# Performance work log

Measured on AMD Instinct MI355X. Metric: run time of the kernel, lower is better.

Reference implementation:

```python
import jax, jax.numpy as jnp
import numpy as np

B, H, W, C = 32, 64, 64, 256


def setup_inputs() -> dict:
    key = jax.random.key(0)
    kq, kk, kv = jax.random.split(key, 3)
    query = jax.random.normal(kq, (B, H, W, C), dtype=jnp.float32)
    keys = jax.random.normal(kk, (B, H, W, C), dtype=jnp.float32)
    values = jax.random.normal(kv, (B, H, W, C), dtype=jnp.float32)
    return {"query": query, "keys": keys, "values": values}


def reference(query, keys, values):
    # A[b,q,k] = sum_{h,w} query[b,h,w,q] * keys[b,h,w,k]
    scores = jnp.einsum("bhwq,bhwk->bqk", query, keys)
    attn = jax.nn.softmax(scores, axis=-1)  # softmax over keys axis
    # out[b,q,h,w] = sum_k attn[b,q,k] * values[b,h,w,k]
    out = jnp.einsum("bqk,bhwk->bqhw", attn, values)
    return out
```

## Files before the change

kernel.cpp:

```cpp
#include <hip/hip_runtime.h>
#include <hip/hip_bf16.h>

#define B_  32
#define HW_ 4096
#define C_  256
#define S_LDS 40

using bf16x8 = __attribute__((ext_vector_type(8))) short;
using f32x4  = __attribute__((ext_vector_type(4))) float;

__device__ __forceinline__ ushort f2bf_rn(float x) {
    uint u = __builtin_bit_cast(uint, x);
    u += 0x7FFFu + ((u >> 16) & 1u);
    return (ushort)(u >> 16);
}
__device__ __forceinline__ uint pk_bf2(float a, float b) {
    return ((uint)f2bf_rn(b) << 16) | (uint)f2bf_rn(a);
}
__device__ __forceinline__ uint pk_rtz(float x0, float x1) {
    return __builtin_amdgcn_perm(__builtin_bit_cast(uint, x1),
                                 __builtin_bit_cast(uint, x0), 0x07060302u);
}
__device__ __forceinline__ void split2_rtz(float x0, float x1, uint& hi2, uint& lo2) {
    uint u0 = __builtin_bit_cast(uint, x0), u1 = __builtin_bit_cast(uint, x1);
    hi2 = __builtin_amdgcn_perm(u1, u0, 0x07060302u);
    float h0 = __builtin_bit_cast(float, u0 & 0xFFFF0000u);
    float h1 = __builtin_bit_cast(float, u1 & 0xFFFF0000u);
    lo2 = pk_rtz(x0 - h0, x1 - h1);
}

__global__ __launch_bounds__(256) void scores_kernel(const float* __restrict__ qg,
                                                     const float* __restrict__ kg,
                                                     float* __restrict__ scores) {
    int x  = blockIdx.x;
    int s  = x & 3;
    int tn = (x >> 2) & 3;
    int tm = (x >> 4) & 1;
    int b  = x >> 5;

    __shared__ __align__(16) ushort Qhi[128 * S_LDS], Qlo[128 * S_LDS];
    __shared__ __align__(16) ushort Khi[64 * S_LDS],  Klo[64 * S_LDS];

    int tid = threadIdx.x, lane = tid & 63, w = tid >> 6;
    int m0 = (w >> 1) * 64;
    int n0 = (w & 1) * 32;
    int g = lane >> 4, r16 = lane & 15;

    int cq = tid & 127;
    int hq = (tid >> 7) * 16;
    int ck = tid & 63;
    int hk = (tid >> 6) * 8;

    const float* qcol = qg + (size_t)b * HW_ * C_ + tm * 128 + cq;
    const float* kcol = kg + (size_t)b * HW_ * C_ + tn * 64 + ck;

    f32x4 acc[4][2];
#pragma unroll
    for (int i = 0; i < 4; ++i)
#pragma unroll
        for (int j = 0; j < 2; ++j) acc[i][j] = (f32x4){0.f, 0.f, 0.f, 0.f};

#define LOAD_QK(qr, kr, itv) {                                                 \
        int hw0 = s * 1024 + (itv) * 32;                                       \
        const float* qp = qcol + (size_t)(hw0 + hq) * C_;                      \
        _Pragma("unroll")                                                      \
        for (int j = 0; j < 16; ++j) qr[j] = qp[(size_t)j * C_];               \
        const float* kp = kcol + (size_t)(hw0 + hk) * C_;                      \
        _Pragma("unroll")                                                      \
        for (int j = 0; j < 8; ++j) kr[j] = kp[(size_t)j * C_];                \
    }

#define CONVERT_STORE(qr, kr) {                                                \
        uint qh[8], ql[8];                                                     \
        _Pragma("unroll")                                                      \
        for (int p = 0; p < 8; ++p) split2_rtz(qr[2*p], qr[2*p+1], qh[p], ql[p]); \
        int qb_ = cq * S_LDS + hq;                                             \
        *reinterpret_cast<uint4*>(&Qhi[qb_])     = make_uint4(qh[0], qh[1], qh[2], qh[3]); \
        *reinterpret_cast<uint4*>(&Qhi[qb_ + 8]) = make_uint4(qh[4], qh[5], qh[6], qh[7]); \
        *reinterpret_cast<uint4*>(&Qlo[qb_])     = make_uint4(ql[0], ql[1], ql[2], ql[3]); \
        *reinterpret_cast<uint4*>(&Qlo[qb_ + 8]) = make_uint4(ql[4], ql[5], ql[6], ql[7]); \
        uint kh[4], kl[4];                                                     \
        _Pragma("unroll")                                                      \
        for (int p = 0; p < 4; ++p) split2_rtz(kr[2*p], kr[2*p+1], kh[p], kl[p]); \
        int kb_ = ck * S_LDS + hk;                                             \
        *reinterpret_cast<uint4*>(&Khi[kb_]) = make_uint4(kh[0], kh[1], kh[2], kh[3]); \
        *reinterpret_cast<uint4*>(&Klo[kb_]) = make_uint4(kl[0], kl[1], kl[2], kl[3]); \
    }

#define MFMA_PHASE() {                                                         \
        bf16x8 ahi[4], alo[4];                                                 \
        _Pragma("unroll")                                                      \
        for (int mi = 0; mi < 4; ++mi) {                                       \
            int off = (m0 + mi * 16 + r16) * S_LDS + g * 8;                    \
            ahi[mi] = *reinterpret_cast<const bf16x8*>(&Qhi[off]);             \
            alo[mi] = *reinterpret_cast<const bf16x8*>(&Qlo[off]);             \
        }                                                                      \
        _Pragma("unroll")                                                      \
        for (int ni = 0; ni < 2; ++ni) {                                       \
            int off = (n0 + ni * 16 + r16) * S_LDS + g * 8;                    \
            bf16x8 bhi = *reinterpret_cast<const bf16x8*>(&Khi[off]);          \
            bf16x8 blo = *reinterpret_cast<const bf16x8*>(&Klo[off]);          \
            _Pragma("unroll")                                                  \
            for (int mi = 0; mi < 4; ++mi) {                                   \
                acc[mi][ni] = __builtin_amdgcn_mfma_f32_16x16x32_bf16(ahi[mi], bhi, acc[mi][ni], 0, 0, 0); \
                acc[mi][ni] = __builtin_amdgcn_mfma_f32_16x16x32_bf16(ahi[mi], blo, acc[mi][ni], 0, 0, 0); \
                acc[mi][ni] = __builtin_amdgcn_mfma_f32_16x16x32_bf16(alo[mi], bhi, acc[mi][ni], 0, 0, 0); \
            }                                                                  \
        }                                                                      \
    }

#define STEP(qc, kc, qn, kn, itv, doload) {                                    \
        if (doload) LOAD_QK(qn, kn, (itv) + 1);                                \
        __syncthreads();                                                       \
        CONVERT_STORE(qc, kc);                                                 \
        __syncthreads();                                                       \
        MFMA_PHASE();                                                          \
    }

    float qa[16], ka[8], qb[16], kb[8];
    LOAD_QK(qa, ka, 0);
    for (int p = 0; p < 16; ++p) {
        STEP(qa, ka, qb, kb, 2 * p, true);
        STEP(qb, kb, qa, ka, 2 * p + 1, p < 15);
    }

#pragma unroll
    for (int mi = 0; mi < 4; ++mi)
#pragma unroll
        for (int ni = 0; ni < 2; ++ni)
#pragma unroll
            for (int r = 0; r < 4; ++r) {
                int qrow = tm * 128 + m0 + mi * 16 + g * 4 + r;
                int kc   = tn * 64 + n0 + ni * 16 + r16;
                atomicAdd(&scores[((size_t)b * 256 + qrow) * 256 + kc], acc[mi][ni][r]);
            }
#undef STEP
#undef MFMA_PHASE
#undef CONVERT_STORE
#undef LOAD_QK
}

__global__ __launch_bounds__(256) void softmax_kernel(const float* __restrict__ scores,
                                                      ushort* __restrict__ attn) {
    int wid  = blockIdx.x * 4 + (threadIdx.x >> 6);
    int lane = threadIdx.x & 63;
    const float4 v = *reinterpret_cast<const float4*>(scores + (size_t)wid * 256 + lane * 4);
    float m = fmaxf(fmaxf(v.x, v.y), fmaxf(v.z, v.w));
#pragma unroll
    for (int off = 32; off; off >>= 1) m = fmaxf(m, __shfl_xor(m, off, 64));
    float e0 = __expf(v.x - m), e1 = __expf(v.y - m), e2 = __expf(v.z - m), e3 = __expf(v.w - m);
    float ssum = e0 + e1 + e2 + e3;
#pragma unroll
    for (int off = 32; off; off >>= 1) ssum += __shfl_xor(ssum, off, 64);
    float inv = 1.0f / ssum;
    uint2 o;
    o.x = pk_bf2(e0 * inv, e1 * inv);
    o.y = pk_bf2(e2 * inv, e3 * inv);
    *reinterpret_cast<uint2*>(attn + (size_t)wid * 256 + lane * 4) = o;
}

__global__ __launch_bounds__(256) void pv_kernel(const ushort* __restrict__ attn,
                                                 const float* __restrict__ vg,
                                                 float* __restrict__ out) {
    int b   = blockIdx.x >> 6;
    int hw0 = (blockIdx.x & 63) * 64;
    int tid = threadIdx.x, lane = tid & 63, w = tid >> 6;
    int m0  = w * 64;
    int g   = lane >> 4, r16 = lane & 15;

    f32x4 acc[4][4];
#pragma unroll
    for (int i = 0; i < 4; ++i)
#pragma unroll
        for (int j = 0; j < 4; ++j) acc[i][j] = (f32x4){0.f, 0.f, 0.f, 0.f};

    for (int ks = 0; ks < 8; ++ks) {
        int k0 = ks * 32;
        bf16x8 a[4];
#pragma unroll
        for (int mi = 0; mi < 4; ++mi) {
            int qrow = m0 + mi * 16 + r16;
            a[mi] = *reinterpret_cast<const bf16x8*>(attn + ((size_t)b * 256 + qrow) * 256 + k0 + g * 8);
        }
        float4 vv[4][2];
#pragma unroll
        for (int ni = 0; ni < 4; ++ni) {
            int hw = hw0 + ni * 16 + r16;
            const float* vp = vg + ((size_t)(b * HW_ + hw)) * C_ + k0 + g * 8;
            vv[ni][0] = *reinterpret_cast<const float4*>(vp);
            vv[ni][1] = *reinterpret_cast<const float4*>(vp + 4);
        }
#pragma unroll
        for (int ni = 0; ni < 4; ++ni) {
            bf16x8 bf;
            uint* bu = reinterpret_cast<uint*>(&bf);
            bu[0] = pk_rtz(vv[ni][0].x, vv[ni][0].y);
            bu[1] = pk_rtz(vv[ni][0].z, vv[ni][0].w);
            bu[2] = pk_rtz(vv[ni][1].x, vv[ni][1].y);
            bu[3] = pk_rtz(vv[ni][1].z, vv[ni][1].w);
#pragma unroll
            for (int mi = 0; mi < 4; ++mi)
                acc[mi][ni] = __builtin_amdgcn_mfma_f32_16x16x32_bf16(a[mi], bf, acc[mi][ni], 0, 0, 0);
        }
    }

#pragma unroll
    for (int mi = 0; mi < 4; ++mi)
#pragma unroll
        for (int ni = 0; ni < 4; ++ni)
#pragma unroll
            for (int r = 0; r < 4; ++r) {
                int qrow = m0 + mi * 16 + g * 4 + r;
                int hw   = hw0 + ni * 16 + r16;
                out[((size_t)b * 256 + qrow) * 4096 + hw] = acc[mi][ni][r];
            }
}

extern "C" void kernel_launch(void* const* d_in, const int* in_sizes, int n_in,
                              void* d_out, int out_size, void* d_ws, size_t ws_size,
                              hipStream_t stream) {
    const float* q = (const float*)d_in[0];
    const float* k = (const float*)d_in[1];
    const float* v = (const float*)d_in[2];
    float* out = (float*)d_out;

    float*  scores = (float*)d_ws;
    ushort* attn   = (ushort*)((char*)d_ws + (size_t)B_ * 256 * 256 * 4);

    (void)hipMemsetAsync(d_ws, 0, (size_t)B_ * 256 * 256 * 4, stream);
    scores_kernel<<<1024, 256, 0, stream>>>(q, k, scores);
    softmax_kernel<<<2048, 256, 0, stream>>>(scores, attn);
    pv_kernel<<<2048, 256, 0, stream>>>(attn, v, out);
}
```

Measured before the change: 215.3 us.

## Double the split-K blocks in scores and stage V through swizzled LDS in PV

```diff
diff --git a/kernel.cpp b/kernel.cpp
--- a/kernel.cpp
+++ b/kernel.cpp
@@ -8,6 +8,7 @@
 
 using bf16x8 = __attribute__((ext_vector_type(8))) short;
 using f32x4  = __attribute__((ext_vector_type(4))) float;
+using u32x4  = __attribute__((ext_vector_type(4))) uint;
 
 __device__ __forceinline__ ushort f2bf_rn(float x) {
     uint u = __builtin_bit_cast(uint, x);
@@ -29,14 +30,14 @@
     lo2 = pk_rtz(x0 - h0, x1 - h1);
 }
 
-__global__ __launch_bounds__(256) void scores_kernel(const float* __restrict__ qg,
-                                                     const float* __restrict__ kg,
-                                                     float* __restrict__ scores) {
+__global__ __launch_bounds__(256, 4) void scores_kernel(const float* __restrict__ qg,
+                                                        const float* __restrict__ kg,
+                                                        float* __restrict__ scores) {
     int x  = blockIdx.x;
-    int s  = x & 3;
-    int tn = (x >> 2) & 3;
-    int tm = (x >> 4) & 1;
-    int b  = x >> 5;
+    int s  = x & 7;
+    int tn = (x >> 3) & 3;
+    int tm = (x >> 5) & 1;
+    int b  = x >> 6;
 
     __shared__ __align__(16) ushort Qhi[128 * S_LDS], Qlo[128 * S_LDS];
     __shared__ __align__(16) ushort Khi[64 * S_LDS],  Klo[64 * S_LDS];
@@ -61,7 +62,7 @@
         for (int j = 0; j < 2; ++j) acc[i][j] = (f32x4){0.f, 0.f, 0.f, 0.f};
 
 #define LOAD_QK(qr, kr, itv) {                                                 \
-        int hw0 = s * 1024 + (itv) * 32;                                       \
+        int hw0 = s * 512 + (itv) * 32;                                        \
         const float* qp = qcol + (size_t)(hw0 + hq) * C_;                      \
         _Pragma("unroll")                                                      \
         for (int j = 0; j < 16; ++j) qr[j] = qp[(size_t)j * C_];               \
@@ -75,19 +76,20 @@
         _Pragma("unroll")                                                      \
         for (int p = 0; p < 8; ++p) split2_rtz(qr[2*p], qr[2*p+1], qh[p], ql[p]); \
         int qb_ = cq * S_LDS + hq;                                             \
-        *reinterpret_cast<uint4*>(&Qhi[qb_])     = make_uint4(qh[0], qh[1], qh[2], qh[3]); \
-        *reinterpret_cast<uint4*>(&Qhi[qb_ + 8]) = make_uint4(qh[4], qh[5], qh[6], qh[7]); \
-        *reinterpret_cast<uint4*>(&Qlo[qb_])     = make_uint4(ql[0], ql[1], ql[2], ql[3]); \
-        *reinterpret_cast<uint4*>(&Qlo[qb_ + 8]) = make_uint4(ql[4], ql[5], ql[6], ql[7]); \
+        *reinterpret_cast<u32x4*>(&Qhi[qb_])     = (u32x4){qh[0], qh[1], qh[2], qh[3]}; \
+        *reinterpret_cast<u32x4*>(&Qhi[qb_ + 8]) = (u32x4){qh[4], qh[5], qh[6], qh[7]}; \
+        *reinterpret_cast<u32x4*>(&Qlo[qb_])     = (u32x4){ql[0], ql[1], ql[2], ql[3]}; \
+        *reinterpret_cast<u32x4*>(&Qlo[qb_ + 8]) = (u32x4){ql[4], ql[5], ql[6], ql[7]}; \
         uint kh[4], kl[4];                                                     \
         _Pragma("unroll")                                                      \
         for (int p = 0; p < 4; ++p) split2_rtz(kr[2*p], kr[2*p+1], kh[p], kl[p]); \
         int kb_ = ck * S_LDS + hk;                                             \
-        *reinterpret_cast<uint4*>(&Khi[kb_]) = make_uint4(kh[0], kh[1], kh[2], kh[3]); \
-        *reinterpret_cast<uint4*>(&Klo[kb_]) = make_uint4(kl[0], kl[1], kl[2], kl[3]); \
+        *reinterpret_cast<u32x4*>(&Khi[kb_]) = (u32x4){kh[0], kh[1], kh[2], kh[3]}; \
+        *reinterpret_cast<u32x4*>(&Klo[kb_]) = (u32x4){kl[0], kl[1], kl[2], kl[3]}; \
     }
 
 #define MFMA_PHASE() {                                                         \
+        __builtin_amdgcn_s_setprio(1);                                         \
         bf16x8 ahi[4], alo[4];                                                 \
         _Pragma("unroll")                                                      \
         for (int mi = 0; mi < 4; ++mi) {                                       \
@@ -107,6 +109,7 @@
                 acc[mi][ni] = __builtin_amdgcn_mfma_f32_16x16x32_bf16(alo[mi], bhi, acc[mi][ni], 0, 0, 0); \
             }                                                                  \
         }                                                                      \
+        __builtin_amdgcn_s_setprio(0);                                         \
     }
 
 #define STEP(qc, kc, qn, kn, itv, doload) {                                    \
@@ -119,9 +122,9 @@
 
     float qa[16], ka[8], qb[16], kb[8];
     LOAD_QK(qa, ka, 0);
-    for (int p = 0; p < 16; ++p) {
+    for (int p = 0; p < 8; ++p) {
         STEP(qa, ka, qb, kb, 2 * p, true);
-        STEP(qb, kb, qa, ka, 2 * p + 1, p < 15);
+        STEP(qb, kb, qa, ka, 2 * p + 1, p < 7);
     }
 
 #pragma unroll
@@ -159,48 +162,72 @@
     *reinterpret_cast<uint2*>(attn + (size_t)wid * 256 + lane * 4) = o;
 }
 
-__global__ __launch_bounds__(256) void pv_kernel(const ushort* __restrict__ attn,
-                                                 const float* __restrict__ vg,
-                                                 float* __restrict__ out) {
+__global__ __launch_bounds__(256, 4) void pv_kernel(const ushort* __restrict__ attn,
+                                                    const float* __restrict__ vg,
+                                                    float* __restrict__ out) {
     int b   = blockIdx.x >> 6;
     int hw0 = (blockIdx.x & 63) * 64;
     int tid = threadIdx.x, lane = tid & 63, w = tid >> 6;
     int m0  = w * 64;
     int g   = lane >> 4, r16 = lane & 15;
 
+    __shared__ __align__(16) float Vt[2 * 64 * 32];
+
+    int srow = tid >> 2;
+    int sslot = (tid & 3) * 2;
+    int wi0 = srow * 32 + ((sslot ^ (srow & 7)) * 4);
+    int wi1 = srow * 32 + (((sslot + 1) ^ (srow & 7)) * 4);
+    const float* vstage = vg + ((size_t)(b * HW_ + hw0 + srow)) * C_ + sslot * 4;
+
+    const ushort* abase = attn + (size_t)b * 256 * 256 + g * 8;
+
     f32x4 acc[4][4];
 #pragma unroll
     for (int i = 0; i < 4; ++i)
 #pragma unroll
         for (int j = 0; j < 4; ++j) acc[i][j] = (f32x4){0.f, 0.f, 0.f, 0.f};
 
-    for (int ks = 0; ks < 8; ++ks) {
-        int k0 = ks * 32;
+    {
+        f32x4 p0 = *reinterpret_cast<const f32x4*>(vstage);
+        f32x4 p1 = *reinterpret_cast<const f32x4*>(vstage + 4);
+        *reinterpret_cast<f32x4*>(&Vt[wi0]) = p0;
+        *reinterpret_cast<f32x4*>(&Vt[wi1]) = p1;
+    }
+    __syncthreads();
+
+    for (int p = 0; p < 8; ++p) {
+        float* rbuf = &Vt[(p & 1) * 64 * 32];
+        float* wbuf = &Vt[((p + 1) & 1) * 64 * 32];
+
+        f32x4 n0v, n1v;
+        if (p < 7) {
+            n0v = *reinterpret_cast<const f32x4*>(vstage + (p + 1) * 32);
+            n1v = *reinterpret_cast<const f32x4*>(vstage + (p + 1) * 32 + 4);
+        }
+
+        int k0 = p * 32;
         bf16x8 a[4];
 #pragma unroll
-        for (int mi = 0; mi < 4; ++mi) {
-            int qrow = m0 + mi * 16 + r16;
-            a[mi] = *reinterpret_cast<const bf16x8*>(attn + ((size_t)b * 256 + qrow) * 256 + k0 + g * 8);
-        }
-        float4 vv[4][2];
+        for (int mi = 0; mi < 4; ++mi)
+            a[mi] = *reinterpret_cast<const bf16x8*>(abase + (size_t)(m0 + mi * 16 + r16) * 256 + k0);
+
 #pragma unroll
         for (int ni = 0; ni < 4; ++ni) {
-            int hw = hw0 + ni * 16 + r16;
-            const float* vp = vg + ((size_t)(b * HW_ + hw)) * C_ + k0 + g * 8;
-            vv[ni][0] = *reinterpret_cast<const float4*>(vp);
-            vv[ni][1] = *reinterpret_cast<const float4*>(vp + 4);
-        }
-#pragma unroll
-        for (int ni = 0; ni < 4; ++ni) {
-            bf16x8 bf;
-            uint* bu = reinterpret_cast<uint*>(&bf);
-            bu[0] = pk_rtz(vv[ni][0].x, vv[ni][0].y);
-            bu[1] = pk_rtz(vv[ni][0].z, vv[ni][0].w);
-            bu[2] = pk_rtz(vv[ni][1].x, vv[ni][1].y);
-            bu[3] = pk_rtz(vv[ni][1].z, vv[ni][1].w);
+            int row = ni * 16 + r16, key = row & 7;
+            f32x4 f0 = *reinterpret_cast<const f32x4*>(&rbuf[row * 32 + (((2 * g)     ^ key) * 4)]);
+            f32x4 f1 = *reinterpret_cast<const f32x4*>(&rbuf[row * 32 + (((2 * g + 1) ^ key) * 4)]);
+            bf16x8 bf = __builtin_bit_cast(bf16x8, (u32x4){
+                pk_rtz(f0[0], f0[1]), pk_rtz(f0[2], f0[3]),
+                pk_rtz(f1[0], f1[1]), pk_rtz(f1[2], f1[3])});
 #pragma unroll
             for (int mi = 0; mi < 4; ++mi)
                 acc[mi][ni] = __builtin_amdgcn_mfma_f32_16x16x32_bf16(a[mi], bf, acc[mi][ni], 0, 0, 0);
+        }
+
+        if (p < 7) {
+            *reinterpret_cast<f32x4*>(&wbuf[wi0]) = n0v;
+            *reinterpret_cast<f32x4*>(&wbuf[wi1]) = n1v;
+            __syncthreads();
         }
     }
 
@@ -228,7 +255,7 @@
     ushort* attn   = (ushort*)((char*)d_ws + (size_t)B_ * 256 * 256 * 4);
 
     (void)hipMemsetAsync(d_ws, 0, (size_t)B_ * 256 * 256 * 4, stream);
-    scores_kernel<<<1024, 256, 0, stream>>>(q, k, scores);
+    scores_kernel<<<2048, 256, 0, stream>>>(q, k, scores);
     softmax_kernel<<<2048, 256, 0, stream>>>(scores, attn);
     pv_kernel<<<2048, 256, 0, stream>>>(attn, v, out);
 }
```

Result: faster. 181.8 us (-15.5%).
